# Performance work log

Measured on AMD Instinct MI355X. Metric: run time of the kernel, lower is better.

## Reference

```python
import math
import jax, jax.numpy as jnp
import numpy as np

GROUPS = 8
EPS = 1e-5


def setup_inputs() -> dict:
    key = jax.random.key(0)
    ks = jax.random.split(key, 4)
    B, C, H, W = 4, 128, 64, 64
    x = jax.random.normal(ks[0], (B, C, H, W), dtype=jnp.float32)
    norm_w = jnp.ones((C,), dtype=jnp.float32)
    norm_b = jnp.zeros((C,), dtype=jnp.float32)
    qkv_w = jax.random.normal(ks[1], (3 * C, C), dtype=jnp.float32) * 0.02
    qkv_b = jnp.zeros((3 * C,), dtype=jnp.float32)
    proj_w = jax.random.normal(ks[2], (C, C), dtype=jnp.float32) * 0.02
    proj_b = jnp.zeros((C,), dtype=jnp.float32)
    return {"x": x, "norm_w": norm_w, "norm_b": norm_b,
            "qkv_w": qkv_w, "qkv_b": qkv_b,
            "proj_w": proj_w, "proj_b": proj_b}


def reference(x, norm_w, norm_b, qkv_w, qkv_b, proj_w, proj_b):
    B, C, H, W = x.shape
    N = H * W
    # GroupNorm over (C/G, H, W) per group
    xr = x.reshape(B, GROUPS, C // GROUPS, N)
    mean = xr.mean(axis=(2, 3), keepdims=True)
    var = xr.var(axis=(2, 3), keepdims=True)
    h = ((xr - mean) * jax.lax.rsqrt(var + EPS)).reshape(B, C, N)
    h = h * norm_w[None, :, None] + norm_b[None, :, None]
    # 1x1 conv QKV == per-pixel linear: [B, 3C, N]
    qkv = jnp.einsum('oc,bcn->bon', qkv_w, h) + qkv_b[None, :, None]
    q, k, v = jnp.split(qkv, 3, axis=1)  # each [B, C, N]
    scale = 1.0 / math.sqrt(C)
    attn = jax.nn.softmax(jnp.einsum('bci,bcj->bij', q, k) * scale, axis=-1)  # [B,N,N]
    out = jnp.einsum('bij,bcj->bci', attn, v)  # [B, C, N]
    proj = jnp.einsum('oc,bcn->bon', proj_w, out) + proj_b[None, :, None]
    return x + proj.reshape(B, C, H, W)
```

## Files before the change

### kernel.cpp

```cpp
#include <hip/hip_runtime.h>

typedef float  f32x4   __attribute__((ext_vector_type(4)));
typedef float  f32x16  __attribute__((ext_vector_type(16)));
typedef short  bf16x8  __attribute__((ext_vector_type(8)));
typedef unsigned short u16;

constexpr int B_ = 4;
constexpr int C_ = 128;
constexpr int N_ = 4096;
constexpr int G_ = 8;
constexpr int CperG = 16;
constexpr float EPS_ = 1e-5f;
constexpr float SCALE_ = 0.08838834764831845f;

__device__ inline u16 f2bf(float f) {
    union { float f; unsigned u; } v; v.f = f;
    unsigned r = v.u + 0x7fffu + ((v.u >> 16) & 1u);
    return (u16)(r >> 16);
}
__device__ inline unsigned pk2(float a, float b) {
    return (unsigned)f2bf(a) | ((unsigned)f2bf(b) << 16);
}
__device__ inline void gload16(const u16* g, u16* l) {
    __builtin_amdgcn_global_load_lds(
        (const __attribute__((address_space(1))) void*)g,
        (__attribute__((address_space(3))) void*)l, 16, 0, 0);
}

__global__ __launch_bounds__(256) void prep_kernel(const float* __restrict__ x,
                                                   const float* __restrict__ qw,
                                                   const float* __restrict__ pw,
                                                   float* __restrict__ stats2,
                                                   u16* __restrict__ qwbf,
                                                   u16* __restrict__ pwbf) {
    int blk = blockIdx.x;
    if (blk < 256) {
        __shared__ float rs[4], rss[4];
        int bg = blk >> 3, chunk = blk & 7;
        const float4* xp = (const float4*)(x + (size_t)bg * (CperG * N_)) + chunk * 2048;
        float s = 0.f, ss = 0.f;
        for (int i = threadIdx.x; i < 2048; i += 256) {
            float4 v = xp[i];
            s  += v.x + v.y + v.z + v.w;
            ss += v.x*v.x + v.y*v.y + v.z*v.z + v.w*v.w;
        }
        #pragma unroll
        for (int off = 32; off > 0; off >>= 1) {
            s  += __shfl_down(s, off);
            ss += __shfl_down(ss, off);
        }
        int wv = threadIdx.x >> 6, ln = threadIdx.x & 63;
        if (ln == 0) { rs[wv] = s; rss[wv] = ss; }
        __syncthreads();
        if (threadIdx.x == 0) {
            stats2[blk*2]     = rs[0] + rs[1] + rs[2] + rs[3];
            stats2[blk*2 + 1] = rss[0] + rss[1] + rss[2] + rss[3];
        }
    } else {
        int fidx = ((blk - 256) * 256 + threadIdx.x) * 4;
        float4 v;
        u16* dst;
        if (fidx < 3*C_*C_) { v = *(const float4*)(qw + fidx); dst = qwbf + fidx; }
        else { int j = fidx - 3*C_*C_; v = *(const float4*)(pw + j); dst = pwbf + j; }
        ushort4 o;
        o.x = f2bf(v.x); o.y = f2bf(v.y); o.z = f2bf(v.z); o.w = f2bf(v.w);
        *(ushort4*)dst = o;
    }
}

constexpr int HS = 136;

__global__ __launch_bounds__(256, 2) void qkv_kernel(const float* __restrict__ x,
                                                     const float* __restrict__ stats2,
                                                     const float* __restrict__ nw,
                                                     const float* __restrict__ nb,
                                                     const u16* __restrict__ qwbf,
                                                     const float* __restrict__ qb,
                                                     u16* __restrict__ Qt,
                                                     u16* __restrict__ Kt,
                                                     u16* __restrict__ Vb,
                                                     float* __restrict__ qn2,
                                                     int* __restrict__ kmaxI) {
    int n0 = (blockIdx.x & 63) * 64;
    int b  = blockIdx.x >> 6;
    __shared__ u16 hs[64 * HS];
    __shared__ u16 Wl[64 * HS];
    __shared__ float gmean[8], grstd[8];
    int t = threadIdx.x;
    const float invM = 1.f / (float)(CperG * N_);
    if (t < 8) {
        const float* sp = stats2 + (size_t)(b*G_ + t)*16;
        float S = 0.f, SS = 0.f;
        #pragma unroll
        for (int k2 = 0; k2 < 8; ++k2) { S += sp[k2*2]; SS += sp[k2*2 + 1]; }
        float mean = S * invM;
        gmean[t] = mean;
        grstd[t] = rsqrtf(SS * invM - mean*mean + EPS_);
    }
    __syncthreads();
    #pragma unroll
    for (int r = 0; r < 8; ++r) {
        int idx = t + (r << 8);
        int c = idx >> 4, n4 = idx & 15;
        int g = c >> 4;
        float wgt = nw[c] * grstd[g];
        float bia = nb[c] - gmean[g] * wgt;
        float4 xv = *(const float4*)(x + ((size_t)(b*C_ + c))*N_ + n0 + n4*4);
        int base = (n4*4) * HS + c;
        hs[base         ] = f2bf(xv.x*wgt + bia);
        hs[base +     HS] = f2bf(xv.y*wgt + bia);
        hs[base + 2 * HS] = f2bf(xv.z*wgt + bia);
        hs[base + 3 * HS] = f2bf(xv.w*wgt + bia);
    }
    __syncthreads();
    int w = t >> 6, lane = t & 63, lo = lane & 15, hi = lane >> 4;
    bf16x8 hf[4];
    #pragma unroll
    for (int ch = 0; ch < 4; ++ch)
        hf[ch] = *(const bf16x8*)(hs + (16*w + lo)*HS + 32*ch + 8*hi);

    float nq = 0.f, nk = 0.f;
    for (int ck = 0; ck < 6; ++ck) {
        {
            int r = t >> 2, p = t & 3;
            const u16* src = qwbf + (size_t)(ck*64 + r)*C_ + p*32;
            u16* dst = Wl + r*HS + p*32;
            #pragma unroll
            for (int k2 = 0; k2 < 4; ++k2)
                *(uint4*)(dst + 8*k2) = *(const uint4*)(src + 8*k2);
        }
        __syncthreads();
        #pragma unroll
        for (int ot = 0; ot < 4; ++ot) {
            int o16 = ck*64 + ot*16;
            bf16x8 wf[4];
            #pragma unroll
            for (int ch = 0; ch < 4; ++ch)
                wf[ch] = *(const bf16x8*)(Wl + (ot*16 + lo)*HS + 32*ch + 8*hi);
            if (o16 < 2*C_) {
                f32x4 acc = (f32x4){0.f, 0.f, 0.f, 0.f};
                #pragma unroll
                for (int ch = 0; ch < 4; ++ch)
                    acc = __builtin_amdgcn_mfma_f32_16x16x32_bf16(wf[ch], hf[ch], acc, 0, 0, 0);
                float4 bv = *(const float4*)(qb + o16 + 4*hi);
                int n = n0 + 16*w + lo;
                ushort4 o4;
                if (o16 < C_) {
                    float q0 = (acc[0] + bv.x) * SCALE_;
                    float q1 = (acc[1] + bv.y) * SCALE_;
                    float q2 = (acc[2] + bv.z) * SCALE_;
                    float q3 = (acc[3] + bv.w) * SCALE_;
                    nq += (q0*q0 + q1*q1) + (q2*q2 + q3*q3);
                    o4.x = f2bf(q0); o4.y = f2bf(q1); o4.z = f2bf(q2); o4.w = f2bf(q3);
                    *(ushort4*)(Qt + ((size_t)b*N_ + n)*C_ + o16 + 4*hi) = o4;
                } else {
                    float k0 = acc[0] + bv.x, k1 = acc[1] + bv.y;
                    float k2 = acc[2] + bv.z, k3 = acc[3] + bv.w;
                    nk += (k0*k0 + k1*k1) + (k2*k2 + k3*k3);
                    o4.x = f2bf(k0); o4.y = f2bf(k1); o4.z = f2bf(k2); o4.w = f2bf(k3);
                    *(ushort4*)(Kt + ((size_t)b*N_ + n)*C_ + (o16 - C_) + 4*hi) = o4;
                }
            } else {
                f32x4 acc = (f32x4){0.f, 0.f, 0.f, 0.f};
                #pragma unroll
                for (int ch = 0; ch < 4; ++ch)
                    acc = __builtin_amdgcn_mfma_f32_16x16x32_bf16(hf[ch], wf[ch], acc, 0, 0, 0);
                float bia = qb[o16 + lo];
                ushort4 o4;
                o4.x = f2bf(acc[0] + bia);
                o4.y = f2bf(acc[1] + bia);
                o4.z = f2bf(acc[2] + bia);
                o4.w = f2bf(acc[3] + bia);
                *(ushort4*)(Vb + ((size_t)b*C_ + (o16 - 2*C_) + lo)*N_ + n0 + 16*w + 4*hi) = o4;
            }
        }
        __syncthreads();
    }
    nq += __shfl_xor(nq, 16); nq += __shfl_xor(nq, 32);
    nk += __shfl_xor(nk, 16); nk += __shfl_xor(nk, 32);
    if (lane < 16) qn2[(size_t)b*N_ + n0 + 16*w + lo] = nq;
    #pragma unroll
    for (int off = 1; off < 16; off <<= 1)
        nk = fmaxf(nk, __shfl_xor(nk, off));
    if (lane == 0) atomicMax(&kmaxI[b], __float_as_int(nk));
}

__global__ __launch_bounds__(512, 2) void attn_kernel(const u16* __restrict__ Qt,
                                                      const u16* __restrict__ Kt,
                                                      const u16* __restrict__ Vb,
                                                      const float* __restrict__ qn2,
                                                      const int* __restrict__ kmaxI,
                                                      const u16* __restrict__ pwbf,
                                                      const float* __restrict__ pb,
                                                      const float* __restrict__ x,
                                                      float* __restrict__ out) {
    int lb = blockIdx.x;
    int b  = lb & 3;
    int i0 = 64 * (lb >> 2);
    int t = threadIdx.x;
    int w = t >> 6, lane = t & 63;
    int l31 = lane & 31, l15 = lane & 15, h = lane >> 5;
    int qt = w >> 2, ks = w & 3;

    const u16* Qb = Qt + (size_t)b*N_*C_;
    const u16* Kb = Kt + (size_t)b*N_*C_;
    const u16* Vv = Vb + (size_t)b*C_*N_;

    __shared__ __align__(16) u16 KV[2][32768];
    __shared__ float lW[8][32];
    float* Ob = (float*)KV;

    float kmax = sqrtf(__int_as_float(kmaxI[b]));
    float mq = sqrtf(qn2[(size_t)b*N_ + i0 + 32*qt + l31]) * kmax * 1.02f + 1e-6f;

    bf16x8 qf[8];
    #pragma unroll
    for (int ch = 0; ch < 8; ++ch)
        qf[ch] = *(const bf16x8*)(Qb + (size_t)(i0 + 32*qt + l31)*C_ + 16*ch + 8*h);

    f32x16 acc[4];
    #pragma unroll
    for (int ct = 0; ct < 4; ++ct)
        #pragma unroll
        for (int r = 0; r < 16; ++r) acc[ct][r] = 0.f;
    float psum = 0.f;

    int srow = lane >> 4, schnk = lane & 15;

    auto stage = [&](int tile0, u16* buf) {
        if (w < 4) {
            #pragma unroll
            for (int j = 0; j < 8; ++j) {
                int k0 = 32*w + 4*j;
                int r  = k0 + srow;
                gload16(Kb + (size_t)(tile0 + r)*C_ + (schnk ^ (r & 15))*8, buf + k0*128);
            }
        } else {
            #pragma unroll
            for (int j = 0; j < 8; ++j) {
                int c0 = 32*(w - 4) + 4*j;
                int ch = c0 + srow;
                gload16(Vv + (size_t)ch*N_ + tile0 + (schnk ^ (ch & 15))*8,
                        buf + 16384 + c0*128);
            }
        }
    };

    stage(0, KV[0]);
    __syncthreads();

    for (int it = 0; it < 32; ++it) {
        int cur = it & 1;
        if (it < 31) stage((it + 1) * 128, KV[cur ^ 1]);
        u16* Kl = KV[cur];
        u16* Vl = KV[cur] + 16384;
        f32x16 s;
        #pragma unroll
        for (int r = 0; r < 16; ++r) s[r] = 0.f;
        int krow = (32*ks + l31) * 128;
        #pragma unroll
        for (int ch = 0; ch < 8; ++ch) {
            bf16x8 kf = *(const bf16x8*)(Kl + krow + ((2*ch + h) ^ l15)*8);
            s = __builtin_amdgcn_mfma_f32_32x32x16_bf16(kf, qf[ch], s, 0, 0, 0);
        }
        float p[16];
        #pragma unroll
        for (int r = 0; r < 16; ++r) {
            p[r] = __expf(s[r] - mq);
            psum += p[r];
        }
        union { bf16x8 v; unsigned u[4]; } pf1, pf2;
        pf1.u[0] = pk2(p[0],  p[1]);  pf1.u[1] = pk2(p[2],  p[3]);
        pf1.u[2] = pk2(p[4],  p[5]);  pf1.u[3] = pk2(p[6],  p[7]);
        pf2.u[0] = pk2(p[8],  p[9]);  pf2.u[1] = pk2(p[10], p[11]);
        pf2.u[2] = pk2(p[12], p[13]); pf2.u[3] = pk2(p[14], p[15]);
        #pragma unroll
        for (int ct = 0; ct < 4; ++ct) {
            int vbase = (32*ct + l31) * 128;
            union { bf16x8 v; long long q[2]; } v1, v2;
            v1.q[0] = *(const long long*)(Vl + vbase + (2*((4*ks    ) ^ l15) + h)*4);
            v1.q[1] = *(const long long*)(Vl + vbase + (2*((4*ks + 1) ^ l15) + h)*4);
            v2.q[0] = *(const long long*)(Vl + vbase + (2*((4*ks + 2) ^ l15) + h)*4);
            v2.q[1] = *(const long long*)(Vl + vbase + (2*((4*ks + 3) ^ l15) + h)*4);
            acc[ct] = __builtin_amdgcn_mfma_f32_32x32x16_bf16(v1.v, pf1.v, acc[ct], 0, 0, 0);
            acc[ct] = __builtin_amdgcn_mfma_f32_32x32x16_bf16(v2.v, pf2.v, acc[ct], 0, 0, 0);
        }
        __syncthreads();
    }

    psum += __shfl_xor(psum, 32);
    if (lane < 32) lW[w][l31] = psum;
    for (int i = 0; i < 4; ++i) {
        if (ks == i) {
            int q = 32*qt + l31;
            #pragma unroll
            for (int ct = 0; ct < 4; ++ct)
                #pragma unroll
                for (int qd = 0; qd < 4; ++qd) {
                    int c = 32*ct + 8*qd + 4*h;
                    float4 vv;
                    vv.x = acc[ct][4*qd + 0];
                    vv.y = acc[ct][4*qd + 1];
                    vv.z = acc[ct][4*qd + 2];
                    vv.w = acc[ct][4*qd + 3];
                    if (i == 0) {
                        *(float4*)(Ob + q*132 + c) = vv;
                    } else {
                        float4 o = *(const float4*)(Ob + q*132 + c);
                        o.x += vv.x; o.y += vv.y; o.z += vv.z; o.w += vv.w;
                        *(float4*)(Ob + q*132 + c) = o;
                    }
                }
        }
        __syncthreads();
    }
    int lo = lane & 15, hi = lane >> 4;
    int qtile = w >> 1, os = w & 1;
    int q = 16*qtile + lo;
    int qg = 4*(q >> 5), qc = q & 31;
    float linv = 1.f / (lW[qg][qc] + lW[qg+1][qc] + lW[qg+2][qc] + lW[qg+3][qc]);
    bf16x8 aa[4];
    #pragma unroll
    for (int ch = 0; ch < 4; ++ch) {
        float4 ua = *(const float4*)(Ob + q*132 + 32*ch + 8*hi);
        float4 ub = *(const float4*)(Ob + q*132 + 32*ch + 8*hi + 4);
        union { bf16x8 hh; unsigned u[4]; } pkd;
        pkd.u[0] = pk2(ua.x*linv, ua.y*linv);
        pkd.u[1] = pk2(ua.z*linv, ua.w*linv);
        pkd.u[2] = pk2(ub.x*linv, ub.y*linv);
        pkd.u[3] = pk2(ub.z*linv, ub.w*linv);
        aa[ch] = pkd.hh;
    }
    #pragma unroll
    for (int ot = 0; ot < 4; ++ot) {
        int ob = 64*os + 16*ot;
        f32x4 pr = (f32x4){0.f, 0.f, 0.f, 0.f};
        #pragma unroll
        for (int ch = 0; ch < 4; ++ch) {
            bf16x8 bw = *(const bf16x8*)(pwbf + (size_t)(ob + lo)*C_ + 32*ch + 8*hi);
            pr = __builtin_amdgcn_mfma_f32_16x16x32_bf16(aa[ch], bw, pr, 0, 0, 0);
        }
        int o = ob + lo;
        float pbv = pb[o];
        size_t base = ((size_t)(b*C_ + o))*N_ + i0 + 16*qtile + 4*hi;
        float4 xr = *(const float4*)(x + base);
        float4 res;
        res.x = xr.x + pr[0] + pbv;
        res.y = xr.y + pr[1] + pbv;
        res.z = xr.z + pr[2] + pbv;
        res.w = xr.w + pr[3] + pbv;
        *(float4*)(out + base) = res;
    }
}

extern "C" void kernel_launch(void* const* d_in, const int* in_sizes, int n_in,
                              void* d_out, int out_size, void* d_ws, size_t ws_size,
                              hipStream_t stream) {
    const float* x  = (const float*)d_in[0];
    const float* nw = (const float*)d_in[1];
    const float* nb = (const float*)d_in[2];
    const float* qw = (const float*)d_in[3];
    const float* qb = (const float*)d_in[4];
    const float* pw = (const float*)d_in[5];
    const float* pb = (const float*)d_in[6];
    float* out = (float*)d_out;

    char* p = (char*)d_ws;
    float* stats2 = (float*)p;                 p += 2048;
    float* qn2    = (float*)p;                 p += (size_t)B_*N_*4;
    int*   kmaxI  = (int*)p;                   p += 256;
    u16*   qwbf   = (u16*)p;                   p += (size_t)3*C_*C_*2;
    u16*   pwbf   = (u16*)p;                   p += (size_t)C_*C_*2;
    u16*   Qt     = (u16*)p;                   p += (size_t)B_*N_*C_*2;
    u16*   Kt     = (u16*)p;                   p += (size_t)B_*N_*C_*2;
    u16*   Vb     = (u16*)p;

    prep_kernel<<<dim3(320), 256, 0, stream>>>(x, qw, pw, stats2, qwbf, pwbf);
    qkv_kernel<<<dim3(256), 256, 0, stream>>>(x, stats2, nw, nb, qwbf, qb,
                                              Qt, Kt, Vb, qn2, kmaxI);
    attn_kernel<<<dim3(256), 512, 0, stream>>>(Qt, Kt, Vb, qn2, kmaxI,
                                               pwbf, pb, x, out);
}
```

Measured before the change: 169.5 us.

## Pre-swizzle K/V into MFMA fragment layout and load directly to registers

The QKV kernel now writes K and V in a fragment-major layout that matches the MFMA operand order. The attention kernel can then load K and V tiles straight from global memory into registers, replacing the LDS double-buffered staging and its per-iteration barriers. K for the next step is prefetched into registers. Each wave now reads its K/V fragments from global memory without sharing through LDS, which raises global/L2 traffic and register pressure.

```diff
diff --git a/kernel.cpp b/kernel.cpp
--- a/kernel.cpp
+++ b/kernel.cpp
@@ -20,11 +20,6 @@
 }
 __device__ inline unsigned pk2(float a, float b) {
     return (unsigned)f2bf(a) | ((unsigned)f2bf(b) << 16);
-}
-__device__ inline void gload16(const u16* g, u16* l) {
-    __builtin_amdgcn_global_load_lds(
-        (const __attribute__((address_space(1))) void*)g,
-        (__attribute__((address_space(3))) void*)l, 16, 0, 0);
 }
 
 __global__ __launch_bounds__(256) void prep_kernel(const float* __restrict__ x,
@@ -77,8 +72,8 @@
                                                      const u16* __restrict__ qwbf,
                                                      const float* __restrict__ qb,
                                                      u16* __restrict__ Qt,
-                                                     u16* __restrict__ Kt,
-                                                     u16* __restrict__ Vb,
+                                                     u16* __restrict__ Ksw,
+                                                     u16* __restrict__ Vsw,
                                                      float* __restrict__ qn2,
                                                      int* __restrict__ kmaxI) {
     int n0 = (blockIdx.x & 63) * 64;
@@ -119,6 +114,7 @@
     for (int ch = 0; ch < 4; ++ch)
         hf[ch] = *(const bf16x8*)(hs + (16*w + lo)*HS + 32*ch + 8*hi);
 
+    int Tb = (n0 >> 5) + (w >> 1);
     float nq = 0.f, nk = 0.f;
     for (int ck = 0; ck < 6; ++ck) {
         {
@@ -158,7 +154,10 @@
                     float k2 = acc[2] + bv.z, k3 = acc[3] + bv.w;
                     nk += (k0*k0 + k1*k1) + (k2*k2 + k3*k3);
                     o4.x = f2bf(k0); o4.y = f2bf(k1); o4.z = f2bf(k2); o4.w = f2bf(k3);
-                    *(ushort4*)(Kt + ((size_t)b*N_ + n)*C_ + (o16 - C_) + 4*hi) = o4;
+                    int cc = (o16 - C_) >> 4;
+                    int lp = (16*(w & 1) + lo) + 32*(hi >> 1);
+                    size_t fb = ((size_t)(b*128 + Tb)*8 + cc)*512;
+                    *(ushort4*)(Ksw + fb + lp*8 + 4*(hi & 1)) = o4;
                 }
             } else {
                 f32x4 acc = (f32x4){0.f, 0.f, 0.f, 0.f};
@@ -171,7 +170,11 @@
                 o4.y = f2bf(acc[1] + bia);
                 o4.z = f2bf(acc[2] + bia);
                 o4.w = f2bf(acc[3] + bia);
-                *(ushort4*)(Vb + ((size_t)b*C_ + (o16 - 2*C_) + lo)*N_ + n0 + 16*w + 4*hi) = o4;
+                int m  = (o16 - 2*C_) >> 4;
+                int ct = m >> 1;
+                int lp = (16*(m & 1) + lo) + 32*(hi & 1);
+                size_t fb = (((size_t)(b*4 + ct)*128 + Tb)*2 + (w & 1))*512;
+                *(ushort4*)(Vsw + fb + lp*8 + 4*(hi >> 1)) = o4;
             }
         }
         __syncthreads();
@@ -186,8 +189,8 @@
 }
 
 __global__ __launch_bounds__(512, 2) void attn_kernel(const u16* __restrict__ Qt,
-                                                      const u16* __restrict__ Kt,
-                                                      const u16* __restrict__ Vb,
+                                                      const u16* __restrict__ Ksw,
+                                                      const u16* __restrict__ Vsw,
                                                       const float* __restrict__ qn2,
                                                       const int* __restrict__ kmaxI,
                                                       const u16* __restrict__ pwbf,
@@ -199,24 +202,20 @@
     int i0 = 64 * (lb >> 2);
     int t = threadIdx.x;
     int w = t >> 6, lane = t & 63;
-    int l31 = lane & 31, l15 = lane & 15, h = lane >> 5;
+    int l31 = lane & 31, h = lane >> 5;
     int qt = w >> 2, ks = w & 3;
 
-    const u16* Qb = Qt + (size_t)b*N_*C_;
-    const u16* Kb = Kt + (size_t)b*N_*C_;
-    const u16* Vv = Vb + (size_t)b*C_*N_;
-
-    __shared__ __align__(16) u16 KV[2][32768];
+    __shared__ float Ob[64 * 132];
     __shared__ float lW[8][32];
-    float* Ob = (float*)KV;
 
     float kmax = sqrtf(__int_as_float(kmaxI[b]));
     float mq = sqrtf(qn2[(size_t)b*N_ + i0 + 32*qt + l31]) * kmax * 1.02f + 1e-6f;
 
+    const u16* Qb = Qt + (size_t)b*N_*C_;
     bf16x8 qf[8];
     #pragma unroll
-    for (int ch = 0; ch < 8; ++ch)
-        qf[ch] = *(const bf16x8*)(Qb + (size_t)(i0 + 32*qt + l31)*C_ + 16*ch + 8*h);
+    for (int cc = 0; cc < 8; ++cc)
+        qf[cc] = *(const bf16x8*)(Qb + (size_t)(i0 + 32*qt + l31)*C_ + 16*cc + 8*h);
 
     f32x16 acc[4];
     #pragma unroll
@@ -225,43 +224,32 @@
         for (int r = 0; r < 16; ++r) acc[ct][r] = 0.f;
     float psum = 0.f;
 
-    int srow = lane >> 4, schnk = lane & 15;
-
-    auto stage = [&](int tile0, u16* buf) {
-        if (w < 4) {
+    const u16* Kbase = Ksw + ((size_t)(b*128 + ks*32)*8)*512;
+    bf16x8 kf[8], kn[8];
+    #pragma unroll
+    for (int cc = 0; cc < 8; ++cc)
+        kf[cc] = *(const bf16x8*)(Kbase + cc*512 + lane*8);
+
+    for (int it = 0; it < 32; ++it) {
+        f32x16 s;
+        #pragma unroll
+        for (int r = 0; r < 16; ++r) s[r] = 0.f;
+        #pragma unroll
+        for (int cc = 0; cc < 8; ++cc)
+            s = __builtin_amdgcn_mfma_f32_32x32x16_bf16(kf[cc], qf[cc], s, 0, 0, 0);
+        {
+            const u16* Kn = Kbase + ((size_t)(((it + 1) & 31))*8)*512;
             #pragma unroll
-            for (int j = 0; j < 8; ++j) {
-                int k0 = 32*w + 4*j;
-                int r  = k0 + srow;
-                gload16(Kb + (size_t)(tile0 + r)*C_ + (schnk ^ (r & 15))*8, buf + k0*128);
-            }
-        } else {
-            #pragma unroll
-            for (int j = 0; j < 8; ++j) {
-                int c0 = 32*(w - 4) + 4*j;
-                int ch = c0 + srow;
-                gload16(Vv + (size_t)ch*N_ + tile0 + (schnk ^ (ch & 15))*8,
-                        buf + 16384 + c0*128);
-            }
-        }
-    };
-
-    stage(0, KV[0]);
-    __syncthreads();
-
-    for (int it = 0; it < 32; ++it) {
-        int cur = it & 1;
-        if (it < 31) stage((it + 1) * 128, KV[cur ^ 1]);
-        u16* Kl = KV[cur];
-        u16* Vl = KV[cur] + 16384;
-        f32x16 s;
-        #pragma unroll
-        for (int r = 0; r < 16; ++r) s[r] = 0.f;
-        int krow = (32*ks + l31) * 128;
-        #pragma unroll
-        for (int ch = 0; ch < 8; ++ch) {
-            bf16x8 kf = *(const bf16x8*)(Kl + krow + ((2*ch + h) ^ l15)*8);
-            s = __builtin_amdgcn_mfma_f32_32x32x16_bf16(kf, qf[ch], s, 0, 0, 0);
+            for (int cc = 0; cc < 8; ++cc)
+                kn[cc] = *(const bf16x8*)(Kn + cc*512 + lane*8);
+        }
+        int T = ks*32 + it;
+        bf16x8 v1[4], v2[4];
+        #pragma unroll
+        for (int ct = 0; ct < 4; ++ct) {
+            const u16* vb = Vsw + (((size_t)(b*4 + ct)*128 + T)*2)*512;
+            v1[ct] = *(const bf16x8*)(vb + lane*8);
+            v2[ct] = *(const bf16x8*)(vb + 512 + lane*8);
         }
         float p[16];
         #pragma unroll
@@ -276,16 +264,11 @@
         pf2.u[2] = pk2(p[12], p[13]); pf2.u[3] = pk2(p[14], p[15]);
         #pragma unroll
         for (int ct = 0; ct < 4; ++ct) {
-            int vbase = (32*ct + l31) * 128;
-            union { bf16x8 v; long long q[2]; } v1, v2;
-            v1.q[0] = *(const long long*)(Vl + vbase + (2*((4*ks    ) ^ l15) + h)*4);
-            v1.q[1] = *(const long long*)(Vl + vbase + (2*((4*ks + 1) ^ l15) + h)*4);
-            v2.q[0] = *(const long long*)(Vl + vbase + (2*((4*ks + 2) ^ l15) + h)*4);
-            v2.q[1] = *(const long long*)(Vl + vbase + (2*((4*ks + 3) ^ l15) + h)*4);
-            acc[ct] = __builtin_amdgcn_mfma_f32_32x32x16_bf16(v1.v, pf1.v, acc[ct], 0, 0, 0);
-            acc[ct] = __builtin_amdgcn_mfma_f32_32x32x16_bf16(v2.v, pf2.v, acc[ct], 0, 0, 0);
-        }
-        __syncthreads();
+            acc[ct] = __builtin_amdgcn_mfma_f32_32x32x16_bf16(v1[ct], pf1.v, acc[ct], 0, 0, 0);
+            acc[ct] = __builtin_amdgcn_mfma_f32_32x32x16_bf16(v2[ct], pf2.v, acc[ct], 0, 0, 0);
+        }
+        #pragma unroll
+        for (int cc = 0; cc < 8; ++cc) kf[cc] = kn[cc];
     }
 
     psum += __shfl_xor(psum, 32);
@@ -372,12 +355,12 @@
     u16*   qwbf   = (u16*)p;                   p += (size_t)3*C_*C_*2;
     u16*   pwbf   = (u16*)p;                   p += (size_t)C_*C_*2;
     u16*   Qt     = (u16*)p;                   p += (size_t)B_*N_*C_*2;
-    u16*   Kt     = (u16*)p;                   p += (size_t)B_*N_*C_*2;
-    u16*   Vb     = (u16*)p;
+    u16*   Ksw    = (u16*)p;                   p += (size_t)B_*N_*C_*2;
+    u16*   Vsw    = (u16*)p;
 
     prep_kernel<<<dim3(320), 256, 0, stream>>>(x, qw, pw, stats2, qwbf, pwbf);
     qkv_kernel<<<dim3(256), 256, 0, stream>>>(x, stats2, nw, nb, qwbf, qb,
-                                              Qt, Kt, Vb, qn2, kmaxI);
-    attn_kernel<<<dim3(256), 512, 0, stream>>>(Qt, Kt, Vb, qn2, kmaxI,
+                                              Qt, Ksw, Vsw, qn2, kmaxI);
+    attn_kernel<<<dim3(256), 512, 0, stream>>>(Qt, Ksw, Vsw, qn2, kmaxI,
                                                pwbf, pb, x, out);
 }
```

Result: faster. 152.8 us (-9.8%).
